# Kernel tuning notes

Measured on AMD Instinct MI355X. Metric: run time of the kernel, lower is better.

## Reference

```python
import jax, jax.numpy as jnp
import numpy as np


def setup_inputs() -> dict:
    key = jax.random.key(0)
    k1, k2, k3 = jax.random.split(key, 3)
    B, N, D = 512, 12, 4
    return {
        "x": jax.random.normal(k1, (B, N), dtype=jnp.float32),
        "rys": jax.random.normal(k2, (D, N), dtype=jnp.float32),
        "cnot_params": jax.random.normal(k3, (D, N - 1), dtype=jnp.float32),
    }


def _rx(state, theta, q, B):
    # RX(theta) = [[c, -i s], [-i s, c]], half-angle; theta: (B,)
    s = state.reshape(B, 2 ** q, 2, -1)
    c = jnp.cos(theta * 0.5)[:, None, None].astype(state.dtype)
    sn = (-1j * jnp.sin(theta * 0.5))[:, None, None].astype(state.dtype)
    a0, a1 = s[:, :, 0], s[:, :, 1]
    return jnp.stack([c * a0 + sn * a1, sn * a0 + c * a1], axis=2).reshape(B, -1)


def _ry(state, theta, q, B):
    # RY(theta) = [[c, -s], [s, c]], half-angle; theta: scalar (shared over batch)
    s = state.reshape(B, 2 ** q, 2, -1)
    c = jnp.cos(theta * 0.5).astype(state.dtype)
    sn = jnp.sin(theta * 0.5).astype(state.dtype)
    a0, a1 = s[:, :, 0], s[:, :, 1]
    return jnp.stack([c * a0 - sn * a1, sn * a0 + c * a1], axis=2).reshape(B, -1)


def _cnot(state, q, B):
    # CNOT on adjacent wires (control=q, target=q+1): flip target where control=1
    s = state.reshape(B, 2 ** q, 2, 2, -1)
    return jnp.stack([s[:, :, 0], s[:, :, 1, ::-1]], axis=2).reshape(B, -1)


def reference(x, rys, cnot_params):
    B, n = x.shape
    depth = rys.shape[0]
    # wire 0 is the most-significant bit (PennyLane convention)
    state = jnp.zeros((B, 2 ** n), dtype=jnp.complex64).at[:, 0].set(1.0)
    for q in range(n):
        state = _rx(state, x[:, q], q, B)
    for d in range(depth):
        for q in range(n):
            state = _ry(state, rys[d, q], q, B)
        for q in range(n - 1):  # cnot_params are declared but unused (CNOT is non-parametric)
            state = _cnot(state, q, B)
    probs = jnp.abs(state) ** 2  # (B, 2^n), real
    zs = []
    for q in range(n):
        p = probs.reshape(B, 2 ** q, 2, -1).sum(axis=(1, 3))  # (B, 2)
        zs.append(p[:, 0] - p[:, 1])
    return jnp.stack(zs, axis=1).astype(jnp.float32)  # (B, n)
```

## Files before the change

### kernel.cpp

```cpp
#include <hip/hip_runtime.h>

#define NQ 12
#define DIM 4096
#define BLK 256

typedef float v2f __attribute__((ext_vector_type(2)));

__host__ __device__ constexpr int igrayc(int v) {
    v ^= v >> 1; v ^= v >> 2; v ^= v >> 4; v ^= v >> 8;
    return v & (DIM - 1);
}
__host__ __device__ constexpr int gkf(int v, int k) {
    if (k == 1) v ^= v >> 1;
    else if (k == 2) v ^= v >> 2;
    else { v ^= v >> 2; v ^= v >> 1; }
    return v;
}
__host__ __device__ constexpr int sigf(int v) { return v ^ ((v >> 4) & 15); }
__host__ __device__ constexpr int TkF(int v, int k) { return sigf(gkf(v, k)); }

__device__ __forceinline__ v2f cmul(v2f a, v2f b) {
    v2f r; r.x = a.x * b.x - a.y * b.y; r.y = a.x * b.y + a.y * b.x; return r;
}
__device__ __forceinline__ void gate_pair(v2f& a0, v2f& a1, float c, float s) {
    v2f t0 = a0, t1 = a1;
    a0 = c * t0 - s * t1;
    a1 = s * t0 + c * t1;
}
template<int PB>
__device__ __forceinline__ void gate16(v2f (&a)[16], float c, float s) {
    #pragma unroll
    for (int j0 = 0; j0 < 16; ++j0) {
        if (j0 & PB) continue;
        gate_pair(a[j0], a[j0 | PB], c, s);
    }
}
template<int K, int OSH>
__device__ __forceinline__ void ld16(const char* bufc, int sb8, v2f (&a)[16]) {
    #pragma unroll
    for (int j = 0; j < 16; ++j)
        a[j] = *(const v2f*)(bufc + (sb8 ^ (TkF(j << OSH, K) << 3)));
}
template<int K, int OSH>
__device__ __forceinline__ void st16(char* bufc, int sb8, const v2f (&a)[16]) {
    #pragma unroll
    for (int j = 0; j < 16; ++j)
        *(v2f*)(bufc + (sb8 ^ (TkF(j << OSH, K) << 3))) = a[j];
}

__device__ __forceinline__ float wave64_sum(float v) {
    v += __int_as_float(__builtin_amdgcn_update_dpp(0, __float_as_int(v), 0x111, 0xf, 0xf, true));
    v += __int_as_float(__builtin_amdgcn_update_dpp(0, __float_as_int(v), 0x112, 0xf, 0xf, true));
    v += __int_as_float(__builtin_amdgcn_update_dpp(0, __float_as_int(v), 0x114, 0xf, 0xf, true));
    v += __int_as_float(__builtin_amdgcn_update_dpp(0, __float_as_int(v), 0x118, 0xf, 0xf, true));
    v += __int_as_float(__builtin_amdgcn_update_dpp(0, __float_as_int(v), 0x142, 0xa, 0xf, false));
    v += __int_as_float(__builtin_amdgcn_update_dpp(0, __float_as_int(v), 0x143, 0xc, 0xf, false));
    return v;
}

__global__ __launch_bounds__(BLK, 2)
void qsim_kernel(const float* __restrict__ x,
                 const float* __restrict__ rys,
                 float* __restrict__ out) {
    __shared__ __align__(16) v2f buf[DIM];
    __shared__ float cr[4 * NQ], sr[4 * NQ];
    __shared__ v2f fac[NQ][2];
    __shared__ float zred[4][NQ];

    const int b = blockIdx.x;
    const int t = threadIdx.x;
    char* bufc = (char*)buf;

    if (t < 4 * NQ) {
        float th = 0.5f * rys[t];
        cr[t] = cosf(th); sr[t] = sinf(th);
    }
    if (t >= 64 && t < 64 + NQ) {
        int q = t - 64;
        float xh = 0.5f * x[b * NQ + q];
        float cx = cosf(xh), sx = sinf(xh);
        float th = 0.5f * rys[q];
        float c0 = cosf(th), s0 = sinf(th);
        int p = NQ - 1 - q;
        fac[p][0] = v2f{c0 * cx,  s0 * sx};
        fac[p][1] = v2f{s0 * cx, -c0 * sx};
    }
    __syncthreads();

    const int nbB = (t & 15) | (((t >> 4) & 15) << 8);
    const int nbA7 = ((t & 3) << 4) | (((t >> 2) & 15) << 8)
                   | (((t >> 6) & 3) << 6);

    {
        v2f a[16];
        const int Mb = t ^ (t >> 1);
        v2f P = fac[0][Mb & 1];
        #pragma unroll
        for (int p = 1; p < 7; ++p) P = cmul(P, fac[p][(Mb >> p) & 1]);
        const int b7 = (Mb >> 7) & 1;
        v2f E = cmul(P, fac[7][b7]);
        v2f O = cmul(P, fac[7][b7 ^ 1]);
        v2f L4[4], H4[4];
        #pragma unroll
        for (int v = 0; v < 4; ++v) {
            L4[v] = cmul(fac[8][v & 1],  fac[9][(v >> 1) & 1]);
            H4[v] = cmul(fac[10][v & 1], fac[11][(v >> 1) & 1]);
        }
        #pragma unroll
        for (int j = 0; j < 16; ++j) {
            const int gv = (j ^ (j >> 1)) & 15;
            a[j] = cmul((j & 1) ? O : E, cmul(L4[gv & 3], H4[(gv >> 2) & 3]));
        }
        gate16<1>(a, cr[15], sr[15]);
        gate16<2>(a, cr[14], sr[14]);
        gate16<4>(a, cr[13], sr[13]);
        gate16<8>(a, cr[12], sr[12]);
        st16<1, 8>(bufc, TkF(t, 1) << 3, a);
    }
    __syncthreads();

    #define GATE_PASS(K, NB, OSH, I0, I1, I2, I3)                 \
    {                                                             \
        const int sb8 = TkF(NB, K) << 3;                          \
        v2f a[16];                                                \
        ld16<K, OSH>(bufc, sb8, a);                               \
        gate16<1>(a, cr[I0], sr[I0]);                             \
        gate16<2>(a, cr[I1], sr[I1]);                             \
        gate16<4>(a, cr[I2], sr[I2]);                             \
        gate16<8>(a, cr[I3], sr[I3]);                             \
        st16<K, OSH>(bufc, sb8, a);                               \
    }                                                             \
    __syncthreads();

    GATE_PASS(1, (t << 4), 0, 23, 22, 21, 20)
    GATE_PASS(1, nbB,      4, 19, 18, 17, 16)
    GATE_PASS(2, t,        8, 27, 26, 25, 24)
    GATE_PASS(2, (t << 4), 0, 35, 34, 33, 32)
    GATE_PASS(2, nbB,      4, 31, 30, 29, 28)
    GATE_PASS(3, t,        8, 39, 38, 37, 36)
    GATE_PASS(3, nbA7,     0, 47, 46, 45, 44)
    #undef GATE_PASS

    {
        const int sb8 = TkF(nbB, 3) << 3;
        v2f a[16];
        ld16<3, 4>(bufc, sb8, a);
        gate16<1>(a, cr[43], sr[43]);
        gate16<2>(a, cr[42], sr[42]);
        gate16<4>(a, cr[41], sr[41]);
        gate16<8>(a, cr[40], sr[40]);

        float zacc[NQ];
        #pragma unroll
        for (int q = 0; q < NQ; ++q) zacc[q] = 0.0f;
        #pragma unroll
        for (int j = 0; j < 16; ++j) {
            const int nc = igrayc(j << 4);
            const float pr = a[j].x * a[j].x + a[j].y * a[j].y;
            #pragma unroll
            for (int q = 0; q < NQ; ++q)
                zacc[q] += ((nc >> (NQ - 1 - q)) & 1) ? -pr : pr;
        }
        const int R = igrayc(nbB);
        #pragma unroll
        for (int q = 0; q < NQ; ++q) {
            float v = ((R >> (NQ - 1 - q)) & 1) ? -zacc[q] : zacc[q];
            v = wave64_sum(v);
            if ((t & 63) == 63) zred[t >> 6][q] = v;
        }
    }
    __syncthreads();
    if (t < NQ)
        out[b * NQ + t] = zred[0][t] + zred[1][t] + zred[2][t] + zred[3][t];
}

extern "C" void kernel_launch(void* const* d_in, const int* in_sizes, int n_in,
                              void* d_out, int out_size, void* d_ws, size_t ws_size,
                              hipStream_t stream) {
    const float* x   = (const float*)d_in[0];
    const float* rys = (const float*)d_in[1];
    float* out = (float*)d_out;
    qsim_kernel<<<512, BLK, 0, stream>>>(x, rys, out);
}
```

Measured before the change: 18.00 us.

## Use packed FMA gates, remap LDS pass indices, and Walsh-Hadamard Z reduction

Gate updates are rewritten as vector FMAs on packed float2 with pre-broadcast cos/sin vectors, aiming for packed FMA instructions. Two LDS passes get new per-thread base-index mappings (nbA4, nbA7), likely to cut bank conflicts. The final per-qubit Z accumulation is replaced by a 16-point Walsh-Hadamard butterfly over the probabilities, and each qubit picks one coefficient from it. The index remapping must still cover every amplitude pair exactly once, which is a correctness risk.

```diff
diff --git a/kernel.cpp b/kernel.cpp
--- a/kernel.cpp
+++ b/kernel.cpp
@@ -22,17 +22,18 @@
 __device__ __forceinline__ v2f cmul(v2f a, v2f b) {
     v2f r; r.x = a.x * b.x - a.y * b.y; r.y = a.x * b.y + a.y * b.x; return r;
 }
-__device__ __forceinline__ void gate_pair(v2f& a0, v2f& a1, float c, float s) {
+__device__ __forceinline__ void gate_pair(v2f& a0, v2f& a1, v2f cc, v2f ss, v2f ns) {
     v2f t0 = a0, t1 = a1;
-    a0 = c * t0 - s * t1;
-    a1 = s * t0 + c * t1;
+    a0 = __builtin_elementwise_fma(ns, t1, cc * t0);
+    a1 = __builtin_elementwise_fma(ss, t0, cc * t1);
 }
 template<int PB>
 __device__ __forceinline__ void gate16(v2f (&a)[16], float c, float s) {
+    const v2f cc = {c, c}, ss = {s, s}, ns = {-s, -s};
     #pragma unroll
     for (int j0 = 0; j0 < 16; ++j0) {
         if (j0 & PB) continue;
-        gate_pair(a[j0], a[j0 | PB], c, s);
+        gate_pair(a[j0], a[j0 | PB], cc, ss, ns);
     }
 }
 template<int K, int OSH>
@@ -87,9 +88,12 @@
     }
     __syncthreads();
 
-    const int nbB = (t & 15) | (((t >> 4) & 15) << 8);
-    const int nbA7 = ((t & 3) << 4) | (((t >> 2) & 15) << 8)
-                   | (((t >> 6) & 3) << 6);
+    const int nbB  = (t & 15) | (((t >> 4) & 15) << 8);
+    const int nbA4 = ((t & 3) << 4) | (((t >> 2) & 3) << 8)
+                   | (((t >> 4) & 3) << 6) | (((t >> 6) & 3) << 10);
+    const int nbA7 = ((t & 1) << 4) | (((t >> 1) & 7) << 8)
+                   | (((t >> 4) & 3) << 5) | (((t >> 6) & 1) << 7)
+                   | (((t >> 7) & 1) << 11);
 
     {
         v2f a[16];
@@ -135,7 +139,7 @@
     GATE_PASS(1, (t << 4), 0, 23, 22, 21, 20)
     GATE_PASS(1, nbB,      4, 19, 18, 17, 16)
     GATE_PASS(2, t,        8, 27, 26, 25, 24)
-    GATE_PASS(2, (t << 4), 0, 35, 34, 33, 32)
+    GATE_PASS(2, nbA4,     0, 35, 34, 33, 32)
     GATE_PASS(2, nbB,      4, 31, 30, 29, 28)
     GATE_PASS(3, t,        8, 39, 38, 37, 36)
     GATE_PASS(3, nbA7,     0, 47, 46, 45, 44)
@@ -150,21 +154,29 @@
         gate16<4>(a, cr[41], sr[41]);
         gate16<8>(a, cr[40], sr[40]);
 
-        float zacc[NQ];
+        float pr[16];
         #pragma unroll
-        for (int q = 0; q < NQ; ++q) zacc[q] = 0.0f;
+        for (int j = 0; j < 16; ++j)
+            pr[j] = a[j].x * a[j].x + a[j].y * a[j].y;
         #pragma unroll
-        for (int j = 0; j < 16; ++j) {
-            const int nc = igrayc(j << 4);
-            const float pr = a[j].x * a[j].x + a[j].y * a[j].y;
+        for (int bit = 1; bit < 16; bit <<= 1) {
             #pragma unroll
-            for (int q = 0; q < NQ; ++q)
-                zacc[q] += ((nc >> (NQ - 1 - q)) & 1) ? -pr : pr;
+            for (int j = 0; j < 16; ++j) {
+                if (j & bit) continue;
+                float u = pr[j], w = pr[j | bit];
+                pr[j] = u + w;
+                pr[j | bit] = u - w;
+            }
         }
         const int R = igrayc(nbB);
         #pragma unroll
         for (int q = 0; q < NQ; ++q) {
-            float v = ((R >> (NQ - 1 - q)) & 1) ? -zacc[q] : zacc[q];
+            const int l = NQ - 1 - q;
+            const float cf = (l <= 4) ? pr[15]
+                           : (l == 5) ? pr[14]
+                           : (l == 6) ? pr[12]
+                           : (l == 7) ? pr[8]  : pr[0];
+            float v = ((R >> l) & 1) ? -cf : cf;
             v = wave64_sum(v);
             if ((t & 63) == 63) zred[t >> 6][q] = v;
         }
```

Measured after the change: 17.20 us. 1.05x faster.
